# Optimization experiments

Measured on AMD Instinct MI355X. Metric: run time of the kernel, lower is better.

The kernel has to match this reference:

```python
import jax, jax.numpy as jnp
import numpy as np

NUM_HEADS = 12

def setup_inputs() -> dict:
    key = jax.random.key(0)
    ks = jax.random.split(key, 8)
    B, N, C = 8, 1024, 768
    H = NUM_HEADS
    return {
        "x": jax.random.normal(ks[0], (B, N, C), dtype=jnp.float32),
        "relative_position_index": jax.random.randint(ks[1], (N, N), 0, 2048, dtype=jnp.int64),
        "qkv_weight": jax.random.normal(ks[2], (3 * C, C), dtype=jnp.float32) * 0.02,
        "q_bias": jax.random.normal(ks[3], (C,), dtype=jnp.float32) * 0.02,
        "v_bias": jax.random.normal(ks[4], (C,), dtype=jnp.float32) * 0.02,
        "proj_weight": jax.random.normal(ks[5], (C, C), dtype=jnp.float32) * 0.02,
        "proj_bias": jax.random.normal(ks[6], (C,), dtype=jnp.float32) * 0.02,
        "rel_pos_bias_table": jax.random.normal(ks[7], (2048, H), dtype=jnp.float32) * 0.02,
    }

def reference(x, relative_position_index, qkv_weight, q_bias, v_bias, proj_weight, proj_bias, rel_pos_bias_table):
    B, N, C = x.shape
    H = NUM_HEADS
    d = C // H
    scale = d ** (-0.5)
    # qkv bias: (q_bias, zeros, v_bias) as in the torch module
    qkv_b = jnp.concatenate([q_bias, jnp.zeros_like(v_bias), v_bias])
    qkv = x @ qkv_weight.T + qkv_b  # [B,N,3C]
    qkv = qkv.reshape(B, N, 3, H, d).transpose(2, 0, 3, 1, 4)  # [3,B,H,N,d]
    q, k, v = qkv[0], qkv[1], qkv[2]
    attn = jnp.einsum("bhnd,bhmd->bhnm", q * scale, k)  # [B,H,N,N]
    # relative position bias: table lookup [N,N,H] -> [H,N,N]
    bias = rel_pos_bias_table[relative_position_index].transpose(2, 0, 1)
    attn = attn + bias[None]
    attn = jax.nn.softmax(attn, axis=-1)
    out = jnp.einsum("bhnm,bhmd->bhnd", attn, v)  # [B,H,N,d]
    out = out.transpose(0, 2, 1, 3).reshape(B, N, C)
    return out @ proj_weight.T + proj_bias
```

## Files before the change

### kernel.cpp

```cpp
#include <hip/hip_runtime.h>

typedef unsigned short ushort_t;
typedef __bf16 bf16x8 __attribute__((ext_vector_type(8)));
typedef float f32x4 __attribute__((ext_vector_type(4)));
typedef unsigned int u32x4 __attribute__((ext_vector_type(4)));

#define MFMA(a, b, c) __builtin_amdgcn_mfma_f32_16x16x32_bf16((a), (b), (c), 0, 0, 0)

#define BATCH 8
#define SEQ 1024
#define CDIM 768
#define NH 12
#define HD 64
#define MTOT (BATCH * SEQ)
#define THREEC (3 * CDIM)
#define KVB 64
#define LOG2E 1.44269504088896f

__device__ __forceinline__ ushort_t f2bf(float f) {
    unsigned int u = __builtin_bit_cast(unsigned int, f);
    u = (u + 0x7FFFu + ((u >> 16) & 1u)) >> 16;
    return (ushort_t)u;
}
__device__ __forceinline__ float bf2f(ushort_t b) {
    unsigned int u = ((unsigned int)b) << 16;
    return __builtin_bit_cast(float, u);
}
__device__ __forceinline__ ushort_t bfbits(float f) {
    __bf16 h = (__bf16)f;
    return __builtin_bit_cast(ushort_t, h);
}
__device__ __forceinline__ unsigned int pack2bf(float a, float b) {
    ushort2 p;
    p.x = bfbits(a);
    p.y = bfbits(b);
    return __builtin_bit_cast(unsigned int, p);
}

typedef const __attribute__((address_space(1))) unsigned int* gas_ptr;
typedef __attribute__((address_space(3))) unsigned int* las_ptr;

__device__ __forceinline__ void async16(const ushort_t* g, ushort_t* l) {
    __builtin_amdgcn_global_load_lds((gas_ptr)(const void*)g, (las_ptr)(void*)l, 16, 0, 0);
}

#define WAITVM_(N) asm volatile("s_waitcnt vmcnt(" #N ")" ::: "memory")
#define WAITVM(N) WAITVM_(N)
#define SCHEDB __builtin_amdgcn_sched_barrier(0)

__global__ __launch_bounds__(256) void k_convert(const float* __restrict__ x,
                                                 const float* __restrict__ wq,
                                                 const float* __restrict__ wp,
                                                 ushort_t* __restrict__ xb,
                                                 ushort_t* __restrict__ wqb,
                                                 ushort_t* __restrict__ wpb) {
    const int NX = MTOT * CDIM / 4;
    const int NQ = THREEC * CDIM / 4;
    const int NP = CDIM * CDIM / 4;
    int i = blockIdx.x * 256 + threadIdx.x;
    const float4* src;
    ushort_t* dst;
    int off;
    if (i < NX) { src = (const float4*)x; dst = xb; off = i; }
    else if (i < NX + NQ) { src = (const float4*)wq; dst = wqb; off = i - NX; }
    else if (i < NX + NQ + NP) { src = (const float4*)wp; dst = wpb; off = i - NX - NQ; }
    else return;
    float4 v = src[off];
    ushort4 o;
    o.x = f2bf(v.x); o.y = f2bf(v.y); o.z = f2bf(v.z); o.w = f2bf(v.w);
    ((ushort4*)dst)[off] = o;
}

__global__ __launch_bounds__(256) void k_bias(const int* __restrict__ rpi,
                                              const float* __restrict__ table,
                                              ushort_t* __restrict__ biasF) {
    __shared__ int idx_s[16][64];
    int tr = blockIdx.x;
    int tcq = blockIdx.y;
    int t = threadIdx.x;
    {
        int r = t >> 4;
        int c4 = (t & 15) * 4;
        int4 v = *(const int4*)&rpi[(tr * 16 + r) * SEQ + tcq * 64 + c4];
        *(int4*)&idx_s[r][c4] = v;
    }
    __syncthreads();
    int j = t >> 6;
    int lane = t & 63;
    int lq = lane >> 4, l15 = lane & 15;
    int tc = tcq * 4 + j;
    int id[4];
#pragma unroll
    for (int rr = 0; rr < 4; rr++) id[rr] = idx_s[l15][j * 16 + lq * 4 + rr];
#pragma unroll
    for (int h = 0; h < NH; h++) {
        ushort4 o;
        o.x = f2bf(table[id[0] * NH + h] * LOG2E);
        o.y = f2bf(table[id[1] * NH + h] * LOG2E);
        o.z = f2bf(table[id[2] * NH + h] * LOG2E);
        o.w = f2bf(table[id[3] * NH + h] * LOG2E);
        *(ushort4*)&biasF[(((h * 64 + tr) * 64 + tc) * 256 + lane * 4)] = o;
    }
}

template <int MODE>
__global__ __launch_bounds__(256) void k_gemm(const ushort_t* __restrict__ A,
                                              const ushort_t* __restrict__ Bw,
                                              const float* __restrict__ biasq,
                                              const float* __restrict__ biasv,
                                              const float* __restrict__ biasp,
                                              ushort_t* __restrict__ qb,
                                              ushort_t* __restrict__ kb,
                                              ushort_t* __restrict__ vT,
                                              float* __restrict__ outp) {
    __shared__ __attribute__((aligned(16))) ushort_t As[128 * 64];
    __shared__ __attribute__((aligned(16))) ushort_t Bs[128 * 64];
    const int K = CDIM;
    int tid = threadIdx.x, wave = tid >> 6, lane = tid & 63;
    int l15 = lane & 15, lq = lane >> 4;
    int wm = wave >> 1, wn = wave & 1;
    int rowBase = blockIdx.y * 128;
    int colBase = blockIdx.x * 128;
    f32x4 acc[4][4] = {};
    int srow = wave * 8 + (lane >> 3);
    int scol = (((lane & 7) ^ (srow & 7))) * 8;
    int l7 = l15 & 7;
    for (int k0 = 0; k0 < K; k0 += 64) {
#pragma unroll
        for (int is = 0; is < 4; is++) {
            async16(A + (rowBase + is * 32 + srow) * K + k0 + scol,
                    As + is * 2048 + tid * 8);
            async16(Bw + (colBase + is * 32 + srow) * K + k0 + scol,
                    Bs + is * 2048 + tid * 8);
        }
        asm volatile("s_waitcnt vmcnt(0)" ::: "memory");
        __syncthreads();
#pragma unroll
        for (int kk = 0; kk < 64; kk += 32) {
            bf16x8 af[4], bfr[4];
#pragma unroll
            for (int mf = 0; mf < 4; mf++)
                af[mf] = *(const bf16x8*)&As[(wm * 64 + mf * 16 + l15) * 64 +
                                             ((((kk >> 3) + lq) ^ l7) * 8)];
#pragma unroll
            for (int nf = 0; nf < 4; nf++)
                bfr[nf] = *(const bf16x8*)&Bs[(wn * 64 + nf * 16 + l15) * 64 +
                                              ((((kk >> 3) + lq) ^ l7) * 8)];
#pragma unroll
            for (int mf = 0; mf < 4; mf++)
#pragma unroll
                for (int nf = 0; nf < 4; nf++)
                    acc[mf][nf] = MFMA(af[mf], bfr[nf], acc[mf][nf]);
        }
        __syncthreads();
    }
#pragma unroll
    for (int mf = 0; mf < 4; mf++) {
#pragma unroll
        for (int nf = 0; nf < 4; nf++) {
            int jc = colBase + wn * 64 + nf * 16 + l15;
            int mg0 = rowBase + wm * 64 + mf * 16 + (lane >> 4) * 4;
            if (MODE == 0) {
                int which = jc / CDIM;
                int co = jc - which * CDIM;
                int b = mg0 >> 10, tok0 = mg0 & 1023;
                int hh = co >> 6, dd = co & 63;
                int bh = b * NH + hh;
                if (which == 0) {
                    float bq_ = biasq[co];
#pragma unroll
                    for (int r = 0; r < 4; r++)
                        qb[(bh * SEQ + tok0 + r) * HD + dd] =
                            f2bf((acc[mf][nf][r] + bq_) * 0.125f);
                } else if (which == 1) {
#pragma unroll
                    for (int r = 0; r < 4; r++)
                        kb[(bh * SEQ + tok0 + r) * HD + dd] = f2bf(acc[mf][nf][r]);
                } else {
                    float bv = biasv[co];
                    ushort4 pk;
                    pk.x = f2bf(acc[mf][nf][0] + bv);
                    pk.y = f2bf(acc[mf][nf][1] + bv);
                    pk.z = f2bf(acc[mf][nf][2] + bv);
                    pk.w = f2bf(acc[mf][nf][3] + bv);
                    *(ushort4*)&vT[(size_t)(bh * HD + dd) * SEQ + tok0] = pk;
                }
            } else {
                float bp_ = biasp[jc];
#pragma unroll
                for (int r = 0; r < 4; r++)
                    outp[(size_t)(mg0 + r) * CDIM + jc] = acc[mf][nf][r] + bp_;
            }
        }
    }
}

__global__ __launch_bounds__(256, 4) void k_attn(const ushort_t* __restrict__ qb,
                                                 const ushort_t* __restrict__ kb,
                                                 const ushort_t* __restrict__ vT,
                                                 const ushort_t* __restrict__ biasF,
                                                 ushort_t* __restrict__ ctx) {
    __shared__ __attribute__((aligned(16))) ushort_t Ks[2][KVB * 64];
    __shared__ __attribute__((aligned(16))) ushort_t Vs[2][KVB * 64];

    int lin = ((int)blockIdx.x & 7) * 192 + ((int)blockIdx.x >> 3);
    int h = lin >> 7;
    int b = (lin >> 4) & 7;
    int qt = lin & 15;
    int bh = b * NH + h;
    int tid = threadIdx.x, w = tid >> 6, lane = tid & 63;
    int l15 = lane & 15, lq = lane >> 4, lq4 = lq * 4;
    int row0 = qt * 64 + w * 16;
    int qtile0 = row0 >> 4;

    const ushort_t* qp = qb + bh * SEQ * HD;
    const ushort_t* kp = kb + bh * SEQ * HD;
    const ushort_t* vp = vT + bh * HD * SEQ;
    const ushort_t* bfp = biasF + (size_t)(h * 64 + qtile0) * 64 * 256;

    int lamA = l15 + 32 * (lq & 1);
    int lamB = lamA + 16;

    int rk0, sk0, rk1, sk1;
    {
        int cid0 = tid;
        rk0 = cid0 >> 3; sk0 = ((cid0 & 7) ^ (rk0 & 7)) * 8;
        int cid1 = 256 + tid;
        rk1 = cid1 >> 3; sk1 = ((cid1 & 7) ^ (rk1 & 7)) * 8;
    }

#define STAGE_K(BUF, C0)                                                    \
    do {                                                                    \
        async16(kp + ((C0) + rk0) * HD + sk0, &Ks[BUF][tid * 8]);           \
        async16(kp + ((C0) + rk1) * HD + sk1, &Ks[BUF][(256 + tid) * 8]);   \
    } while (0)
#define STAGE_V(BUF, C0)                                                    \
    do {                                                                    \
        async16(vp + rk0 * SEQ + (C0) + sk0, &Vs[BUF][tid * 8]);            \
        async16(vp + rk1 * SEQ + (C0) + sk1, &Vs[BUF][(256 + tid) * 8]);    \
    } while (0)

    STAGE_K(0, 0); STAGE_V(0, 0); STAGE_K(1, KVB); STAGE_V(1, KVB);

    bf16x8 qfr0 = *(const bf16x8*)&qp[(row0 + l15) * HD + 8 * lq];
    bf16x8 qfr1 = *(const bf16x8*)&qp[(row0 + l15) * HD + 32 + 8 * lq];

    f32x4 Oa[4] = {};
    float mi = -1e30f, li = 0.0f;
    f32x4 accA[4], accB[4];
    unsigned int u0[4][2];

#define QK_BLOCK(AN, KN)                                                       \
    do {                                                                       \
        __builtin_amdgcn_s_setprio(1);                                         \
        _Pragma("unroll") for (int n = 0; n < 4; n++) {                        \
            int krow = n * 16 + l15;                                           \
            bf16x8 kf0 = *(const bf16x8*)&(KN)[krow * 64 + ((lq ^ (krow & 7)) * 8)]; \
            bf16x8 kf1 = *(const bf16x8*)&(KN)[krow * 64 + (((lq + 4) ^ (krow & 7)) * 8)]; \
            f32x4 z0 = {};                                                     \
            z0 = MFMA(kf0, qfr0, z0); z0 = MFMA(kf1, qfr1, z0);                \
            (AN)[n] = z0;                                                      \
        }                                                                      \
        __builtin_amdgcn_s_setprio(0);                                         \
    } while (0)

#define SOFTMAX_STEP(ACC, BFR)                                                 \
    do {                                                                       \
        f32x4 z[4];                                                            \
        _Pragma("unroll") for (int n = 0; n < 4; n++) {                        \
            z[n][0] = fmaf((ACC)[n][0], LOG2E, bf2f((BFR)[n].x));              \
            z[n][1] = fmaf((ACC)[n][1], LOG2E, bf2f((BFR)[n].y));              \
            z[n][2] = fmaf((ACC)[n][2], LOG2E, bf2f((BFR)[n].z));              \
            z[n][3] = fmaf((ACC)[n][3], LOG2E, bf2f((BFR)[n].w));              \
        }                                                                      \
        float tm;                                                              \
        {                                                                      \
            f32x4 mv;                                                          \
            _Pragma("unroll") for (int j = 0; j < 4; j++)                      \
                mv[j] = fmaxf(fmaxf(z[0][j], z[1][j]), fmaxf(z[2][j], z[3][j])); \
            tm = fmaxf(fmaxf(mv[0], mv[1]), fmaxf(mv[2], mv[3]));              \
        }                                                                      \
        tm = fmaxf(tm, __shfl_xor(tm, 16));                                    \
        tm = fmaxf(tm, __shfl_xor(tm, 32));                                    \
        if (!__all(tm <= mi + 8.0f)) {                                         \
            float mn = fmaxf(mi, tm);                                          \
            float al = exp2f(mi - mn);                                         \
            mi = mn; li *= al;                                                 \
            _Pragma("unroll") for (int r = 0; r < 4; r++) {                    \
                float alr = __shfl(al, (lane & 48) | (lq4 + r));               \
                Oa[0][r] *= alr; Oa[1][r] *= alr;                              \
                Oa[2][r] *= alr; Oa[3][r] *= alr;                              \
            }                                                                  \
        }                                                                      \
        f32x4 sv = {};                                                         \
        _Pragma("unroll") for (int n = 0; n < 4; n++) {                        \
            z[n][0] = exp2f(z[n][0] - mi); z[n][1] = exp2f(z[n][1] - mi);      \
            z[n][2] = exp2f(z[n][2] - mi); z[n][3] = exp2f(z[n][3] - mi);      \
            sv += z[n];                                                        \
        }                                                                      \
        float s = (sv[0] + sv[1]) + (sv[2] + sv[3]);                           \
        s += __shfl_xor(s, 16);                                                \
        s += __shfl_xor(s, 32);                                                \
        li += s;                                                               \
        _Pragma("unroll") for (int n = 0; n < 4; n++) {                        \
            u0[n][0] = pack2bf(z[n][0], z[n][1]);                              \
            u0[n][1] = pack2bf(z[n][2], z[n][3]);                              \
        }                                                                      \
    } while (0)

#define ASSEMBLE(KS, PF)                                                       \
    do {                                                                       \
        unsigned int a0 = __shfl((int)u0[2 * (KS)][0], lamA);                  \
        unsigned int b0 = __shfl((int)u0[2 * (KS) + 1][0], lamA);              \
        unsigned int a1 = __shfl((int)u0[2 * (KS)][1], lamA);                  \
        unsigned int b1 = __shfl((int)u0[2 * (KS) + 1][1], lamA);              \
        unsigned int a2 = __shfl((int)u0[2 * (KS)][0], lamB);                  \
        unsigned int b2 = __shfl((int)u0[2 * (KS) + 1][0], lamB);              \
        unsigned int a3 = __shfl((int)u0[2 * (KS)][1], lamB);                  \
        unsigned int b3 = __shfl((int)u0[2 * (KS) + 1][1], lamB);              \
        bool hi_ = (lq & 2) != 0;                                              \
        u32x4 qd;                                                              \
        qd[0] = hi_ ? b0 : a0; qd[1] = hi_ ? b1 : a1;                          \
        qd[2] = hi_ ? b2 : a2; qd[3] = hi_ ? b3 : a3;                          \
        (PF) = __builtin_bit_cast(bf16x8, qd);                                 \
    } while (0)

#define PV_BLOCK(VC)                                                           \
    do {                                                                       \
        __builtin_amdgcn_s_setprio(1);                                         \
        _Pragma("unroll") for (int ks = 0; ks < 2; ks++) {                     \
            bf16x8 pfa;                                                        \
            ASSEMBLE(ks, pfa);                                                 \
            _Pragma("unroll") for (int nc = 0; nc < 4; nc++) {                 \
                int vrow = nc * 16 + l15;                                      \
                bf16x8 vf = *(const bf16x8*)&(VC)[vrow * 64 + (((ks * 4 + lq) ^ (vrow & 7)) * 8)]; \
                Oa[nc] = MFMA(pfa, vf, Oa[nc]);                                \
            }                                                                  \
        }                                                                      \
        __builtin_amdgcn_s_setprio(0);                                         \
    } while (0)

#define ITER(T, AC, AN, DO_STAGE, DO_QK)                                       \
    do {                                                                       \
        WAITVM(0);                                                             \
        SCHEDB;                                                                \
        __builtin_amdgcn_s_barrier();                                          \
        SCHEDB;                                                                \
        const int t_ = (T);                                                    \
        ushort4 bfr0[4];                                                       \
        {                                                                      \
            int kt0 = t_ * 4;                                                  \
            _Pragma("unroll") for (int n = 0; n < 4; n++)                      \
                bfr0[n] = *(const ushort4*)&bfp[(kt0 + n) * 256 + lane * 4];   \
        }                                                                      \
        if (DO_STAGE) STAGE_K(t_ & 1, (t_ + 2) * KVB);                         \
        if (DO_QK) QK_BLOCK(AN, Ks[(t_ + 1) & 1]);                             \
        SOFTMAX_STEP(AC, bfr0);                                                \
        PV_BLOCK(Vs[t_ & 1]);                                                  \
        if (DO_STAGE) {                                                        \
            SCHEDB;                                                            \
            __builtin_amdgcn_s_barrier();                                      \
            SCHEDB;                                                            \
            STAGE_V(t_ & 1, (t_ + 2) * KVB);                                   \
        }                                                                      \
    } while (0)

    WAITVM(6);
    SCHEDB;
    __builtin_amdgcn_s_barrier();
    SCHEDB;
    QK_BLOCK(accA, Ks[0]);

#pragma unroll 1
    for (int tt = 0; tt < 14; tt += 2) {
        ITER(tt,     accA, accB, 1, 1);
        ITER(tt + 1, accB, accA, 1, 1);
    }
    ITER(14, accA, accB, 0, 1);
    ITER(15, accB, accA, 0, 0);

    float rli = 1.0f / li;
#pragma unroll
    for (int r = 0; r < 4; r++) {
        float rl = __shfl(rli, (lane & 48) | (lq4 + r));
#pragma unroll
        for (int nc = 0; nc < 4; nc++) {
            ctx[(size_t)(b * SEQ + row0 + lq4 + r) * CDIM + h * HD + nc * 16 + l15] =
                bfbits(Oa[nc][r] * rl);
        }
    }
#undef ITER
#undef PV_BLOCK
#undef ASSEMBLE
#undef SOFTMAX_STEP
#undef QK_BLOCK
#undef STAGE_V
#undef STAGE_K
}

extern "C" void kernel_launch(void* const* d_in, const int* in_sizes, int n_in,
                              void* d_out, int out_size, void* d_ws, size_t ws_size,
                              hipStream_t stream) {
    const float* x = (const float*)d_in[0];
    const int* rpi = (const int*)d_in[1];
    const float* wqkv = (const float*)d_in[2];
    const float* qbias = (const float*)d_in[3];
    const float* vbias = (const float*)d_in[4];
    const float* wproj = (const float*)d_in[5];
    const float* pbias = (const float*)d_in[6];
    const float* table = (const float*)d_in[7];
    float* out = (float*)d_out;

    char* ws = (char*)d_ws;
    ushort_t* xb    = (ushort_t*)(ws + 0);
    ushort_t* wqb   = (ushort_t*)(ws + 12582912);
    ushort_t* wpb   = (ushort_t*)(ws + 16121856);
    ushort_t* qbuf  = (ushort_t*)(ws + 17301504);
    ushort_t* kbuf  = (ushort_t*)(ws + 29884416);
    ushort_t* vTbuf = (ushort_t*)(ws + 42467328);
    ushort_t* ctx   = (ushort_t*)(ws + 55050240);
    ushort_t* biasF = (ushort_t*)(ws + 67633152);

    k_convert<<<8448, 256, 0, stream>>>(x, wqkv, wproj, xb, wqb, wpb);
    k_bias<<<dim3(64, 16), 256, 0, stream>>>(rpi, table, biasF);
    k_gemm<0><<<dim3(THREEC / 128, MTOT / 128), 256, 0, stream>>>(
        xb, wqb, qbias, vbias, nullptr, qbuf, kbuf, vTbuf, nullptr);
    k_attn<<<1536, 256, 0, stream>>>(qbuf, kbuf, vTbuf, biasF, ctx);
    k_gemm<1><<<dim3(CDIM / 128, MTOT / 128), 256, 0, stream>>>(
        ctx, wpb, nullptr, nullptr, pbias, nullptr, nullptr, nullptr, out);
}
```

Before: 170.3 us.

## Single-buffer V tile in attention kernel to cut LDS usage

The V shared-memory tile goes from double to single buffering, and the next V block is staged only after the current PV step and barrier. This cuts LDS per block by a quarter, which may allow more resident blocks per CU. In exchange, the V load now has only one iteration of lead time instead of two, so the wait at the top of each iteration may stall on memory.

```diff
diff --git a/kernel.cpp b/kernel.cpp
--- a/kernel.cpp
+++ b/kernel.cpp
@@ -201,7 +201,7 @@
                                                  const ushort_t* __restrict__ biasF,
                                                  ushort_t* __restrict__ ctx) {
     __shared__ __attribute__((aligned(16))) ushort_t Ks[2][KVB * 64];
-    __shared__ __attribute__((aligned(16))) ushort_t Vs[2][KVB * 64];
+    __shared__ __attribute__((aligned(16))) ushort_t Vs[KVB * 64];
 
     int lin = ((int)blockIdx.x & 7) * 192 + ((int)blockIdx.x >> 3);
     int h = lin >> 7;
@@ -234,13 +234,13 @@
         async16(kp + ((C0) + rk0) * HD + sk0, &Ks[BUF][tid * 8]);           \
         async16(kp + ((C0) + rk1) * HD + sk1, &Ks[BUF][(256 + tid) * 8]);   \
     } while (0)
-#define STAGE_V(BUF, C0)                                                    \
+#define STAGE_V(C0)                                                         \
     do {                                                                    \
-        async16(vp + rk0 * SEQ + (C0) + sk0, &Vs[BUF][tid * 8]);            \
-        async16(vp + rk1 * SEQ + (C0) + sk1, &Vs[BUF][(256 + tid) * 8]);    \
-    } while (0)
-
-    STAGE_K(0, 0); STAGE_V(0, 0); STAGE_K(1, KVB); STAGE_V(1, KVB);
+        async16(vp + rk0 * SEQ + (C0) + sk0, &Vs[tid * 8]);                 \
+        async16(vp + rk1 * SEQ + (C0) + sk1, &Vs[(256 + tid) * 8]);         \
+    } while (0)
+
+    STAGE_K(0, 0); STAGE_V(0); STAGE_K(1, KVB);
 
     bf16x8 qfr0 = *(const bf16x8*)&qp[(row0 + l15) * HD + 8 * lq];
     bf16x8 qfr1 = *(const bf16x8*)&qp[(row0 + l15) * HD + 32 + 8 * lq];
@@ -325,7 +325,7 @@
         (PF) = __builtin_bit_cast(bf16x8, qd);                                 \
     } while (0)
 
-#define PV_BLOCK(VC)                                                           \
+#define PV_BLOCK()                                                             \
     do {                                                                       \
         __builtin_amdgcn_s_setprio(1);                                         \
         _Pragma("unroll") for (int ks = 0; ks < 2; ks++) {                     \
@@ -333,14 +333,14 @@
             ASSEMBLE(ks, pfa);                                                 \
             _Pragma("unroll") for (int nc = 0; nc < 4; nc++) {                 \
                 int vrow = nc * 16 + l15;                                      \
-                bf16x8 vf = *(const bf16x8*)&(VC)[vrow * 64 + (((ks * 4 + lq) ^ (vrow & 7)) * 8)]; \
+                bf16x8 vf = *(const bf16x8*)&Vs[vrow * 64 + (((ks * 4 + lq) ^ (vrow & 7)) * 8)]; \
                 Oa[nc] = MFMA(pfa, vf, Oa[nc]);                                \
             }                                                                  \
         }                                                                      \
         __builtin_amdgcn_s_setprio(0);                                         \
     } while (0)
 
-#define ITER(T, AC, AN, DO_STAGE, DO_QK)                                       \
+#define ITER(T, AC, AN, DO_KST, DO_VST, DO_QK)                                 \
     do {                                                                       \
         WAITVM(0);                                                             \
         SCHEDB;                                                                \
@@ -353,19 +353,19 @@
             _Pragma("unroll") for (int n = 0; n < 4; n++)                      \
                 bfr0[n] = *(const ushort4*)&bfp[(kt0 + n) * 256 + lane * 4];   \
         }                                                                      \
-        if (DO_STAGE) STAGE_K(t_ & 1, (t_ + 2) * KVB);                         \
+        if (DO_KST) STAGE_K(t_ & 1, (t_ + 2) * KVB);                           \
         if (DO_QK) QK_BLOCK(AN, Ks[(t_ + 1) & 1]);                             \
         SOFTMAX_STEP(AC, bfr0);                                                \
-        PV_BLOCK(Vs[t_ & 1]);                                                  \
-        if (DO_STAGE) {                                                        \
+        PV_BLOCK();                                                            \
+        if (DO_VST) {                                                          \
             SCHEDB;                                                            \
             __builtin_amdgcn_s_barrier();                                      \
             SCHEDB;                                                            \
-            STAGE_V(t_ & 1, (t_ + 2) * KVB);                                   \
-        }                                                                      \
-    } while (0)
-
-    WAITVM(6);
+            STAGE_V((t_ + 1) * KVB);                                           \
+        }                                                                      \
+    } while (0)
+
+    WAITVM(2);
     SCHEDB;
     __builtin_amdgcn_s_barrier();
     SCHEDB;
@@ -373,11 +373,11 @@
 
 #pragma unroll 1
     for (int tt = 0; tt < 14; tt += 2) {
-        ITER(tt,     accA, accB, 1, 1);
-        ITER(tt + 1, accB, accA, 1, 1);
-    }
-    ITER(14, accA, accB, 0, 1);
-    ITER(15, accB, accA, 0, 0);
+        ITER(tt,     accA, accB, 1, 1, 1);
+        ITER(tt + 1, accB, accA, 1, 1, 1);
+    }
+    ITER(14, accA, accB, 0, 1, 1);
+    ITER(15, accB, accA, 0, 0, 0);
 
     float rli = 1.0f / li;
 #pragma unroll
```

After: 170.0 us. No clear change (-0.2%).
